# Kernel optimization log

Measured on AMD Instinct MI355X. Metric: run time of the kernel, lower is better.

Reference implementation:

```python
import jax, jax.numpy as jnp
import numpy as np

B, N, D, H = 2, 2048, 1024, 16
HD = D // H  # 64
EPS = 1e-6


def setup_inputs() -> dict:
    key = jax.random.key(0)
    ks = jax.random.split(key, 16)
    rnd = lambda k, shp: jax.random.normal(k, shp, dtype=jnp.float32)
    w = lambda k, i, o: rnd(k, (i, o)) * 0.02  # stored as (in, out); y = x @ W
    return {
        "x": rnd(ks[0], (B, N, D)),
        "emb_B_D": rnd(ks[1], (B, D)),
        "gate": rnd(ks[2], (B, D)),
        "crossattn_emb": rnd(ks[3], (B, 128, D)),
        "rope_emb_L_1_1_D": rnd(ks[4], (N, HD)),
        "Wq1": w(ks[5], D, D), "Wq2": w(ks[6], D, D),
        "Wk1": w(ks[7], D, D), "Wk2": w(ks[8], D, D),
        "Wv": w(ks[9], D, D),
        "Wo": w(ks[10], D, D),
        "Wada1": w(ks[11], D, D),
        "Wada2": w(ks[12], D, 2 * D),
        "bada2": jnp.zeros((2 * D,), dtype=jnp.float32),
    }


def rotate_half(t):
    t1, t2 = jnp.split(t, 2, axis=-1)
    return jnp.concatenate([-t2, t1], axis=-1)


def reference(x, emb_B_D, gate, crossattn_emb, rope_emb_L_1_1_D,
              Wq1, Wq2, Wk1, Wk2, Wv, Wo, Wada1, Wada2, bada2):
    # adaLN modulation: SiLU -> Linear(no bias) -> Linear(bias)
    ada = jax.nn.silu(emb_B_D) @ Wada1 @ Wada2 + bada2          # [B, 2D]
    shift, scale = jnp.split(ada, 2, axis=1)                    # [B, D] each

    # LayerNorm (no affine) + scale/shift
    mu = jnp.mean(x, axis=-1, keepdims=True)
    var = jnp.var(x, axis=-1, keepdims=True)
    xn = (x - mu) * jax.lax.rsqrt(var + EPS)
    xn = xn * (1.0 + scale[:, None, :]) + shift[:, None, :]     # [B, N, D]

    # QKV projections (each to_q/to_k is two stacked linears, to_v one)
    q = xn @ Wq1 @ Wq2
    k = xn @ Wk1 @ Wk2
    v = xn @ Wv
    split_heads = lambda t: t.reshape(B, N, H, HD).transpose(0, 2, 1, 3)  # b h n d
    q, k, v = split_heads(q), split_heads(k), split_heads(v)

    # RoPE
    cos = jnp.cos(rope_emb_L_1_1_D)[None, None]                 # [1,1,N,HD]
    sin = jnp.sin(rope_emb_L_1_1_D)[None, None]
    q = q * cos + rotate_half(q) * sin
    k = k * cos + rotate_half(k) * sin

    # Attention
    sim = jnp.einsum("bhid,bhjd->bhij", q, k) * (HD ** -0.5)
    attn = jax.nn.softmax(sim, axis=-1)
    out = jnp.einsum("bhij,bhjd->bhid", attn, v)
    out = out.transpose(0, 2, 1, 3).reshape(B, N, D) @ Wo

    # Gated residual
    return x + gate[:, None, :] * out
```

## Files before the change

### kernel.cpp

```cpp
#include <hip/hip_runtime.h>
#include <stdint.h>
#include <math.h>

typedef unsigned short u16;
typedef __attribute__((ext_vector_type(8))) short short8;
typedef __attribute__((ext_vector_type(4))) float f32x4;
typedef __attribute__((ext_vector_type(4))) unsigned short u16x4;
typedef __attribute__((ext_vector_type(2))) unsigned int uint2v;

#define DEV static __device__ __forceinline__

DEV u16 f2bf(float f) {
    unsigned u = __builtin_bit_cast(unsigned, f);
    u = u + 0x7fffu + ((u >> 16) & 1u);
    return (u16)(u >> 16);
}
DEV float bf2f(u16 s) { return __builtin_bit_cast(float, ((unsigned)s) << 16); }
DEV float fexp2(float x) {
#if __has_builtin(__builtin_amdgcn_exp2f)
    return __builtin_amdgcn_exp2f(x);
#else
    return __expf(x * 0.69314718056f);
#endif
}
DEV unsigned cvtpk(float a, float b) {
    unsigned w;
    asm("v_cvt_pk_bf16_f32 %0, %1, %2" : "=v"(w) : "v"(a), "v"(b));
    return w;
}
DEV int xcd_swz(int flat, int nwg) {
    int cpx = nwg >> 3;
    return (flat & 7) * cpx + (flat >> 3);
}

DEV void gl_lds16(const u16* g, u16* l) {
#if __has_builtin(__builtin_amdgcn_global_load_lds)
    __builtin_amdgcn_global_load_lds((const __attribute__((address_space(1))) unsigned int*)g,
                                     (__attribute__((address_space(3))) unsigned int*)l, 16, 0, 0);
#else
    *(short8*)l = *(const short8*)g;
#endif
}

DEV void barrier_lgkm() {
    asm volatile("s_waitcnt lgkmcnt(0)" ::: "memory");
    __builtin_amdgcn_sched_barrier(0);
    __builtin_amdgcn_s_barrier();
}


__global__ __launch_bounds__(256) void k_ada1(const float* __restrict__ emb, const float* __restrict__ W,
                                              float* __restrict__ out) {
    int col = blockIdx.x * 64 + (threadIdx.x & 63);
    int b = blockIdx.y;
    int kbase = blockIdx.z * 128 + (threadIdx.x >> 6) * 32;
    float acc = 0.f;
    for (int k = kbase; k < kbase + 32; k++) {
        float e = emb[b * 1024 + k];
        float se = e / (1.f + __expf(-e));
        acc += se * W[(size_t)k * 1024 + col];
    }
    __shared__ float red[4][64];
    red[threadIdx.x >> 6][threadIdx.x & 63] = acc;
    __syncthreads();
    if (threadIdx.x < 64)
        atomicAdd(out + b * 1024 + blockIdx.x * 64 + threadIdx.x,
                  red[0][threadIdx.x] + red[1][threadIdx.x] + red[2][threadIdx.x] + red[3][threadIdx.x]);
}

__global__ __launch_bounds__(256) void k_prep(const float* s0, u16* d0, const float* s1, u16* d1,
                                              const float* s2, u16* d2, const float* s3, u16* d3,
                                              const float* s4, u16* d4, const float* s5, u16* d5,
                                              const float* __restrict__ t_ada, const float* __restrict__ Wada2,
                                              float* __restrict__ ada, const float* __restrict__ rope,
                                              float* __restrict__ cst, float* __restrict__ snt) {
    __shared__ u16 tile[64][65];
    __shared__ float red[4][64];
    if (blockIdx.z == 6) {
        int flat = blockIdx.y * 16 + blockIdx.x;
        int kq = flat >> 6;
        int rest = flat & 63;
        int b = rest >> 5, xb = rest & 31;
        int col = xb * 64 + (threadIdx.x & 63);
        int kbase = kq * 256 + (threadIdx.x >> 6) * 64;
        float acc = 0.f;
        for (int k = kbase; k < kbase + 64; k++)
            acc += t_ada[b * 1024 + k] * Wada2[(size_t)k * 2048 + col];
        red[threadIdx.x >> 6][threadIdx.x & 63] = acc;
        __syncthreads();
        if (threadIdx.x < 64)
            atomicAdd(ada + b * 2048 + xb * 64 + threadIdx.x,
                      red[0][threadIdx.x] + red[1][threadIdx.x] + red[2][threadIdx.x] + red[3][threadIdx.x]);
        return;
    }
    if (blockIdx.z == 7) {
        int flat = blockIdx.y * 16 + blockIdx.x;
        if (flat < 128) {
            int idx = flat * 1024 + threadIdx.x * 4;
            float4 rv = *(const float4*)(rope + idx);
            float4 cv, sv;
            __sincosf(rv.x, &sv.x, &cv.x);
            __sincosf(rv.y, &sv.y, &cv.y);
            __sincosf(rv.z, &sv.z, &cv.z);
            __sincosf(rv.w, &sv.w, &cv.w);
            *(float4*)(cst + idx) = cv;
            *(float4*)(snt + idx) = sv;
        }
        return;
    }
    const float* s; u16* d;
    switch (blockIdx.z) {
        case 0: s = s0; d = d0; break;
        case 1: s = s1; d = d1; break;
        case 2: s = s2; d = d2; break;
        case 3: s = s3; d = d3; break;
        case 4: s = s4; d = d4; break;
        default: s = s5; d = d5; break;
    }
    int k0 = blockIdx.x * 64, n0 = blockIdx.y * 64;
    int tx = threadIdx.x & 63, ty = threadIdx.x >> 6;
    if (blockIdx.z >= 4) {
        #pragma unroll
        for (int i = 0; i < 16; i++) {
            int kk = ty + 4 * i;
            d[(size_t)(k0 + kk) * 1024 + n0 + tx] = f2bf(s[(size_t)(k0 + kk) * 1024 + n0 + tx]);
        }
        return;
    }
    #pragma unroll
    for (int i = 0; i < 16; i++) {
        int kk = ty + 4 * i;
        tile[kk][tx] = f2bf(s[(size_t)(k0 + kk) * 1024 + n0 + tx]);
    }
    __syncthreads();
    #pragma unroll
    for (int i = 0; i < 16; i++) {
        int nn = ty + 4 * i;
        d[(size_t)(n0 + nn) * 1024 + k0 + tx] = tile[tx][nn];
    }
}

__global__ __launch_bounds__(256) void k_ln(const float* __restrict__ x, const float* __restrict__ ada,
                                            const float* __restrict__ bada2, u16* __restrict__ xn) {
    int row = blockIdx.x;
    int b = row >> 11;
    float4 v = ((const float4*)(x + (size_t)row * 1024))[threadIdx.x];
    float s = v.x + v.y + v.z + v.w;
    float ss = v.x * v.x + v.y * v.y + v.z * v.z + v.w * v.w;
    #pragma unroll
    for (int m = 1; m < 64; m <<= 1) { s += __shfl_xor(s, m, 64); ss += __shfl_xor(ss, m, 64); }
    __shared__ float red[2][4];
    int wave = threadIdx.x >> 6, lane = threadIdx.x & 63;
    if (lane == 0) { red[0][wave] = s; red[1][wave] = ss; }
    __syncthreads();
    s = red[0][0] + red[0][1] + red[0][2] + red[0][3];
    ss = red[1][0] + red[1][1] + red[1][2] + red[1][3];
    float mu = s * (1.f / 1024.f);
    float var = ss * (1.f / 1024.f) - mu * mu;
    float rs = rsqrtf(var + 1e-6f);
    int c = threadIdx.x * 4;
    const float* sh = ada + b * 2048;
    const float* sc = ada + b * 2048 + 1024;
    u16x4 r;
    r.x = f2bf((v.x - mu) * rs * (1.f + sc[c + 0] + bada2[1024 + c + 0]) + sh[c + 0] + bada2[c + 0]);
    r.y = f2bf((v.y - mu) * rs * (1.f + sc[c + 1] + bada2[1024 + c + 1]) + sh[c + 1] + bada2[c + 1]);
    r.z = f2bf((v.z - mu) * rs * (1.f + sc[c + 2] + bada2[1024 + c + 2]) + sh[c + 2] + bada2[c + 2]);
    r.w = f2bf((v.w - mu) * rs * (1.f + sc[c + 3] + bada2[1024 + c + 3]) + sh[c + 3] + bada2[c + 3]);
    *(u16x4*)(xn + (size_t)row * 1024 + c) = r;
}

template <int BM, int BN, int MODE>
DEV void gemm_core(const u16* __restrict__ A, const u16* __restrict__ Bt,
                   u16* __restrict__ Cb, float* __restrict__ Cf, u16* __restrict__ Vt,
                   const float* __restrict__ Xres, const float* __restrict__ gate,
                   const float* __restrict__ cst, const float* __restrict__ snt,
                   float scale, int Nn, int K, int m0, int n0) {
    constexpr int MI = BM / 32, NJ = BN / 32;
    constexpr int PA = BM / 64, PB = BN / 64;
    constexpr int LA = BM * 32, LB = BN * 32;
    constexpr int LBUF = LA + LB;
    constexpr int SST = 3 * LBUF;
    constexpr int SM = (MODE == 2 && BM * 132 > SST) ? BM * 132 : SST;
    __shared__ u16 smem[SM];
    int tid = threadIdx.x;
    int lane = tid & 63, wave = tid >> 6;
    int wm = (wave & 1) * (BM / 2), wn = (wave >> 1) * (BN / 2);
    int lr = lane & 15, quad = lane >> 4;
    f32x4 acc[MI][NJ];
    #pragma unroll
    for (int i = 0; i < MI; i++)
        #pragma unroll
        for (int j = 0; j < NJ; j++) acc[i][j] = f32x4{0.f, 0.f, 0.f, 0.f};

    int arow = tid >> 2;
    int achunk = (tid & 3) * 8;
    const u16* ap = A + (size_t)(m0 + arow) * K + achunk;
    const u16* bp = Bt + (size_t)(n0 + arow) * K + achunk;

    auto stage = [&](int it, int d) {
        int koff = it * 32;
        int ab = d * LBUF, bb = d * LBUF + LA;
        #pragma unroll
        for (int p = 0; p < PA; p++)
            gl_lds16(ap + koff + (size_t)(64 * p) * K, smem + ab + (arow + 64 * p) * 32 + achunk);
        #pragma unroll
        for (int p = 0; p < PB; p++)
            gl_lds16(bp + koff + (size_t)(64 * p) * K, smem + bb + (arow + 64 * p) * 32 + achunk);
    };

    stage(0, 0);
    stage(1, 1);
    asm volatile("s_waitcnt vmcnt(%0)" :: "i"(PA + PB) : "memory");
    __builtin_amdgcn_sched_barrier(0);
    __builtin_amdgcn_s_barrier();
    #pragma unroll 1
    for (int it = 0; it < 32; ++it) {
        int cur = it % 3;
        if (it + 2 < 32) stage(it + 2, (it + 2) % 3);
        int ab = cur * LBUF, bb = ab + LA;
        short8 af[MI], bfr[NJ];
        #pragma unroll
        for (int i = 0; i < MI; i++)
            af[i] = *(const short8*)(smem + ab + (wm + i * 16 + lr) * 32 + quad * 8);
        #pragma unroll
        for (int j = 0; j < NJ; j++)
            bfr[j] = *(const short8*)(smem + bb + (wn + j * 16 + lr) * 32 + quad * 8);
        #pragma unroll
        for (int i = 0; i < MI; i++)
            #pragma unroll
            for (int j = 0; j < NJ; j++)
                acc[i][j] = __builtin_amdgcn_mfma_f32_16x16x32_bf16(af[i], bfr[j], acc[i][j], 0, 0, 0);
        if (it + 1 < 32) {
            if (it + 2 < 32)
                asm volatile("s_waitcnt vmcnt(%0)" :: "i"(PA + PB) : "memory");
            else
                asm volatile("s_waitcnt vmcnt(0)" ::: "memory");
            __builtin_amdgcn_sched_barrier(0);
            __builtin_amdgcn_s_barrier();
        }
    }
    __syncthreads();

    if (MODE == 2) {
        if ((n0 + wn) < 2048) {
            #pragma unroll
            for (int i = 0; i < MI; i++)
                #pragma unroll
                for (int jp = 0; jp < 2; jp++)
                    #pragma unroll
                    for (int r = 0; r < 4; r++) {
                        int row = m0 + wm + i * 16 + quad * 4 + r;
                        int n = row & 2047;
                        int d1 = jp * 16 + lr;
                        float c1 = cst[n * 64 + d1],      s1 = snt[n * 64 + d1];
                        float c2 = cst[n * 64 + d1 + 32], s2 = snt[n * 64 + d1 + 32];
                        float x1 = acc[i][jp][r], x2 = acc[i][jp + 2][r];
                        Cb[(size_t)row * Nn + n0 + wn + d1]      = f2bf(x1 * c1 - x2 * s1);
                        Cb[(size_t)row * Nn + n0 + wn + d1 + 32] = f2bf(x2 * c2 + x1 * s2);
                    }
        } else {
            #pragma unroll
            for (int i = 0; i < MI; i++)
                #pragma unroll
                for (int j = 0; j < NJ; j++) {
                    u16x4 w;
                    w.x = f2bf(acc[i][j][0]); w.y = f2bf(acc[i][j][1]);
                    w.z = f2bf(acc[i][j][2]); w.w = f2bf(acc[i][j][3]);
                    *(u16x4*)(&smem[(wn + j * 16 + lr) * 132 + wm + i * 16 + quad * 4]) = w;
                }
            __syncthreads();
            int d = tid >> 1, half = tid & 1;
            int gcol = n0 - 2048 + d;
            int hv = gcol >> 6, dl = gcol & 63;
            int bb2 = m0 >> 11;
            int nloc = (m0 & 2047) + half * 64;
            u16* dst = Vt + ((size_t)((bb2 * 16 + hv) * 64 + dl)) * 2048 + nloc;
            #pragma unroll
            for (int c = 0; c < 8; c++)
                *(short8*)(dst + c * 8) = *(const short8*)(&smem[d * 132 + half * 64 + c * 8]);
        }
        return;
    }
    #pragma unroll
    for (int i = 0; i < MI; i++)
        #pragma unroll
        for (int j = 0; j < NJ; j++)
            #pragma unroll
            for (int r = 0; r < 4; r++) {
                int row = m0 + wm + i * 16 + quad * 4 + r;
                int col = n0 + wn + j * 16 + lr;
                float v = acc[i][j][r];
                if (MODE == 1) {
                    int b = row >> 11;
                    Cf[(size_t)row * Nn + col] = Xres[(size_t)row * Nn + col] + gate[b * 1024 + col] * v;
                } else {
                    Cb[(size_t)row * Nn + col] = f2bf(v * scale);
                }
            }
}

template <int BM, int BN, int MODE, int WPE>
__global__ __launch_bounds__(256, WPE) void gemm_bt(const u16* __restrict__ A, const u16* __restrict__ Bt,
                                                    u16* __restrict__ Cb, float* __restrict__ Cf,
                                                    u16* __restrict__ Vt,
                                                    const float* __restrict__ Xres, const float* __restrict__ gate,
                                                    const float* __restrict__ cst, const float* __restrict__ snt,
                                                    int Nn, int K) {
    int gx = gridDim.x;
    int flat = blockIdx.y * gx + blockIdx.x;
    int swz = xcd_swz(flat, gx * gridDim.y);
    gemm_core<BM, BN, MODE>(A, Bt, Cb, Cf, Vt, Xres, gate, cst, snt, 1.f, Nn, K,
                            (swz / gx) * BM, (swz % gx) * BN);
}

__global__ __launch_bounds__(256, 4) void gemm_fold(const u16* A0, const u16* B0, u16* C0,
                                                    const u16* A1, const u16* B1, u16* C1) {
    const u16* A = blockIdx.z ? A1 : A0;
    const u16* Bt = blockIdx.z ? B1 : B0;
    u16* C = blockIdx.z ? C1 : C0;
    float scale = blockIdx.z ? 1.0f : 0.18033688f;
    int flat = blockIdx.y * 16 + blockIdx.x;
    int swz = xcd_swz(flat, 128);
    gemm_core<128, 64, 0>(A, Bt, C, nullptr, nullptr, nullptr, nullptr, nullptr, nullptr, scale,
                          1024, 1024, (swz >> 4) * 128, (swz & 15) * 64);
}

__global__ __launch_bounds__(512) void k_attn(const u16* __restrict__ qkv, const u16* __restrict__ vt,
                                              u16* __restrict__ aob) {
    __shared__ u16 pool[128 * 72];
    __shared__ u16 Ks[2][64][64];
    __shared__ u16 Vs[2][64][64];
    int flat = blockIdx.y * 16 + blockIdx.x;
    int swz = xcd_swz(flat, 512);
    int q0 = (swz & 15) * 128;
    int bh = swz >> 4; int b = bh >> 4, h = bh & 15;
    int tid = threadIdx.x;
    int lane = tid & 63, wave = tid >> 6;
    int lr = lane & 15, quad = lane >> 4;
    int srow = tid >> 3, scol = (tid & 7) * 8;
    int sg = (((tid & 7) ^ (srow & 7))) * 8;
    int cc[2] = { ((quad ^ (lr & 7))) * 8, (((4 + quad) ^ (lr & 7))) * 8 };
    int qrow = wave * 16 + lr;

    const u16* kp = qkv + ((size_t)(b * 2048 + srow)) * 2048 + 1024 + h * 64 + sg;
    const u16* vp = vt + ((size_t)(bh * 64 + srow)) * 2048 + sg;

    #pragma unroll
    for (int p = 0; p < 2; p++)
        gl_lds16(qkv + ((size_t)(b * 2048 + q0 + srow + 64 * p)) * 2048 + h * 64 + sg,
                 pool + (srow + 64 * p) * 64 + scol);

    short8 krA, vrA, krB, vrB;
    krA = *(const short8*)(kp);
    vrA = *(const short8*)(vp);
    __syncthreads();
    short8 qf[2];
    #pragma unroll
    for (int ks = 0; ks < 2; ks++)
        qf[ks] = *(const short8*)(pool + qrow * 64 + cc[ks]);
    *(short8*)(&Ks[0][srow][scol]) = krA;
    *(short8*)(&Vs[0][srow][scol]) = vrA;
    krB = *(const short8*)(kp + (size_t)64 * 2048);
    vrB = *(const short8*)(vp + 64);
    __syncthreads();

    float l_part = 0.f;
    f32x4 oacc[4];
    #pragma unroll
    for (int dt = 0; dt < 4; dt++) oacc[dt] = f32x4{0.f, 0.f, 0.f, 0.f};

    auto body = [&](int it, int cur, short8& krF, short8& vrF, short8& krH, short8& vrH) {
        if (it < 30) {
            krF = *(const short8*)(kp + (size_t)(it + 2) * 64 * 2048);
            vrF = *(const short8*)(vp + (it + 2) * 64);
        }
        f32x4 st[4];
        #pragma unroll
        for (int ct = 0; ct < 4; ct++) st[ct] = f32x4{0.f, 0.f, 0.f, 0.f};
        #pragma unroll
        for (int ks = 0; ks < 2; ks++) {
            short8 kf[4];
            #pragma unroll
            for (int ct = 0; ct < 4; ct++)
                kf[ct] = *(const short8*)(&Ks[cur][ct * 16 + lr][cc[ks]]);
            __builtin_amdgcn_s_setprio(1);
            #pragma unroll
            for (int ct = 0; ct < 4; ct++)
                st[ct] = __builtin_amdgcn_mfma_f32_16x16x32_bf16(kf[ct], qf[ks], st[ct], 0, 0, 0);
            __builtin_amdgcn_s_setprio(0);
        }
        #pragma unroll
        for (int ct = 0; ct < 4; ct++) {
            float p0 = fexp2(st[ct][0]);
            float p1 = fexp2(st[ct][1]);
            float p2 = fexp2(st[ct][2]);
            float p3 = fexp2(st[ct][3]);
            l_part += (p0 + p1) + (p2 + p3);
            uint2v w; w.x = cvtpk(p0, p1); w.y = cvtpk(p2, p3);
            *(uint2v*)(pool + qrow * 72 + ct * 16 + quad * 4) = w;
        }
        #pragma unroll
        for (int ks = 0; ks < 2; ks++) {
            short8 pf, vf[4];
            pf = *(const short8*)(pool + qrow * 72 + ks * 32 + quad * 8);
            #pragma unroll
            for (int dt = 0; dt < 4; dt++)
                vf[dt] = *(const short8*)(&Vs[cur][dt * 16 + lr][cc[ks]]);
            __builtin_amdgcn_s_setprio(1);
            #pragma unroll
            for (int dt = 0; dt < 4; dt++)
                oacc[dt] = __builtin_amdgcn_mfma_f32_16x16x32_bf16(pf, vf[dt], oacc[dt], 0, 0, 0);
            __builtin_amdgcn_s_setprio(0);
        }
        if (it < 31) {
            int nxt = cur ^ 1;
            *(short8*)(&Ks[nxt][srow][scol]) = krH;
            *(short8*)(&Vs[nxt][srow][scol]) = vrH;
        }
        barrier_lgkm();
    };

    #pragma unroll 1
    for (int it2 = 0; it2 < 16; ++it2) {
        body(2 * it2,     0, krA, vrA, krB, vrB);
        body(2 * it2 + 1, 1, krB, vrB, krA, vrA);
    }

    float l = l_part;
    l += __shfl_xor(l, 16, 64);
    l += __shfl_xor(l, 32, 64);
    float linv[4];
    #pragma unroll
    for (int r = 0; r < 4; r++)
        linv[r] = 1.f / __shfl(l, quad * 4 + r, 64);
    #pragma unroll
    for (int dt = 0; dt < 4; dt++)
        #pragma unroll
        for (int r = 0; r < 4; r++) {
            int row = q0 + wave * 16 + quad * 4 + r;
            aob[((size_t)(b * 2048 + row)) * 1024 + h * 64 + dt * 16 + lr] =
                f2bf(oacc[dt][r] * linv[r]);
        }
}

extern "C" void kernel_launch(void* const* d_in, const int* in_sizes, int n_in,
                              void* d_out, int out_size, void* d_ws, size_t ws_size,
                              hipStream_t stream) {
    const float* x     = (const float*)d_in[0];
    const float* emb   = (const float*)d_in[1];
    const float* gate  = (const float*)d_in[2];
    const float* rope  = (const float*)d_in[4];
    const float* Wq1   = (const float*)d_in[5];
    const float* Wq2   = (const float*)d_in[6];
    const float* Wk1   = (const float*)d_in[7];
    const float* Wk2   = (const float*)d_in[8];
    const float* Wv    = (const float*)d_in[9];
    const float* Wo    = (const float*)d_in[10];
    const float* Wada1 = (const float*)d_in[11];
    const float* Wada2 = (const float*)d_in[12];
    const float* bada2 = (const float*)d_in[13];
    float* out = (float*)d_out;

    char* ws = (char*)d_ws;
    size_t off = 0;
    auto alloc = [&](size_t bytes) { void* p = ws + off; off += (bytes + 255) & ~(size_t)255; return p; };
    float* t_ada = (float*)alloc(2048 * 4);
    float* ada   = (float*)alloc(4096 * 4);
    float* cst   = (float*)alloc((size_t)131072 * 4);
    float* snt   = (float*)alloc((size_t)131072 * 4);
    u16* xn    = (u16*)alloc((size_t)4096 * 1024 * 2);
    u16* Wq1b  = (u16*)alloc((size_t)1024 * 1024 * 2);
    u16* Wk1b  = (u16*)alloc((size_t)1024 * 1024 * 2);
    u16* Wq2t  = (u16*)alloc((size_t)1024 * 1024 * 2);
    u16* Wk2t  = (u16*)alloc((size_t)1024 * 1024 * 2);
    u16* Wot   = (u16*)alloc((size_t)1024 * 1024 * 2);
    u16* WqkvT = (u16*)alloc((size_t)3072 * 1024 * 2);
    u16* qkvb  = (u16*)alloc((size_t)4096 * 2048 * 2);
    u16* vtb   = (u16*)alloc((size_t)4096 * 1024 * 2);
    u16* aob   = (u16*)alloc((size_t)4096 * 1024 * 2);
    (void)ws_size; (void)in_sizes; (void)n_in; (void)out_size;

    hipMemsetAsync(t_ada, 0, 2048 * 4, stream);
    hipMemsetAsync(ada, 0, 4096 * 4, stream);

    k_ada1<<<dim3(16, 2, 8), 256, 0, stream>>>(emb, Wada1, t_ada);

    k_prep<<<dim3(16, 16, 8), 256, 0, stream>>>(Wq2, Wq2t, Wk2, Wk2t,
                                                Wv, WqkvT + (size_t)2048 * 1024, Wo, Wot,
                                                Wq1, Wq1b, Wk1, Wk1b,
                                                t_ada, Wada2, ada, rope, cst, snt);

    k_ln<<<4096, 256, 0, stream>>>(x, ada, bada2, xn);

    gemm_fold<<<dim3(16, 8, 2), 256, 0, stream>>>(Wq2t, Wq1b, WqkvT,
                                                  Wk2t, Wk1b, WqkvT + (size_t)1024 * 1024);

    gemm_bt<128, 128, 2, 4><<<dim3(24, 32), 256, 0, stream>>>(xn, WqkvT, qkvb, nullptr, vtb,
                                                              nullptr, nullptr, cst, snt, 2048, 1024);

    k_attn<<<dim3(16, 32), 512, 0, stream>>>(qkvb, vtb, aob);

    gemm_bt<128, 64, 1, 4><<<dim3(16, 32), 256, 0, stream>>>(aob, Wot, nullptr, out, nullptr, x, gate,
                                                             nullptr, nullptr, 1024, 1024);
}
```

Baseline: 257.2 us.

## Fuse weight-fold GEMM with LayerNorm launch and shrink output GEMM tile

Result: no change. 260.3 us (+1.2%).

```diff
diff --git a/kernel.cpp b/kernel.cpp
--- a/kernel.cpp
+++ b/kernel.cpp
@@ -140,9 +140,167 @@
     }
 }
 
-__global__ __launch_bounds__(256) void k_ln(const float* __restrict__ x, const float* __restrict__ ada,
-                                            const float* __restrict__ bada2, u16* __restrict__ xn) {
-    int row = blockIdx.x;
+template <int BM, int BN, int MODE>
+DEV void gemm_core(const u16* __restrict__ A, const u16* __restrict__ Bt,
+                   u16* __restrict__ Cb, float* __restrict__ Cf, u16* __restrict__ Vt,
+                   const float* __restrict__ Xres, const float* __restrict__ gate,
+                   const float* __restrict__ cst, const float* __restrict__ snt,
+                   float scale, int Nn, int K, int m0, int n0) {
+    constexpr int MI = BM / 32, NJ = BN / 32;
+    constexpr int PA = BM / 64, PB = BN / 64;
+    constexpr int LA = BM * 32, LB = BN * 32;
+    constexpr int LBUF = LA + LB;
+    constexpr int SST = 3 * LBUF;
+    constexpr int SM = (MODE == 2 && BM * 132 > SST) ? BM * 132 : SST;
+    __shared__ u16 smem[SM];
+    int tid = threadIdx.x;
+    int lane = tid & 63, wave = tid >> 6;
+    int wm = (wave & 1) * (BM / 2), wn = (wave >> 1) * (BN / 2);
+    int lr = lane & 15, quad = lane >> 4;
+    f32x4 acc[MI][NJ];
+    #pragma unroll
+    for (int i = 0; i < MI; i++)
+        #pragma unroll
+        for (int j = 0; j < NJ; j++) acc[i][j] = f32x4{0.f, 0.f, 0.f, 0.f};
+
+    int arow = tid >> 2;
+    int achunk = (tid & 3) * 8;
+    const u16* ap = A + (size_t)(m0 + arow) * K + achunk;
+    const u16* bp = Bt + (size_t)(n0 + arow) * K + achunk;
+
+    auto stage = [&](int it, int d) {
+        int koff = it * 32;
+        int ab = d * LBUF, bb = d * LBUF + LA;
+        #pragma unroll
+        for (int p = 0; p < PA; p++)
+            gl_lds16(ap + koff + (size_t)(64 * p) * K, smem + ab + (arow + 64 * p) * 32 + achunk);
+        #pragma unroll
+        for (int p = 0; p < PB; p++)
+            gl_lds16(bp + koff + (size_t)(64 * p) * K, smem + bb + (arow + 64 * p) * 32 + achunk);
+    };
+
+    stage(0, 0);
+    stage(1, 1);
+    asm volatile("s_waitcnt vmcnt(%0)" :: "i"(PA + PB) : "memory");
+    __builtin_amdgcn_sched_barrier(0);
+    __builtin_amdgcn_s_barrier();
+    #pragma unroll 1
+    for (int it = 0; it < 32; ++it) {
+        int cur = it % 3;
+        if (it + 2 < 32) stage(it + 2, (it + 2) % 3);
+        int ab = cur * LBUF, bb = ab + LA;
+        short8 af[MI], bfr[NJ];
+        #pragma unroll
+        for (int i = 0; i < MI; i++)
+            af[i] = *(const short8*)(smem + ab + (wm + i * 16 + lr) * 32 + quad * 8);
+        #pragma unroll
+        for (int j = 0; j < NJ; j++)
+            bfr[j] = *(const short8*)(smem + bb + (wn + j * 16 + lr) * 32 + quad * 8);
+        #pragma unroll
+        for (int i = 0; i < MI; i++)
+            #pragma unroll
+            for (int j = 0; j < NJ; j++)
+                acc[i][j] = __builtin_amdgcn_mfma_f32_16x16x32_bf16(af[i], bfr[j], acc[i][j], 0, 0, 0);
+        if (it + 1 < 32) {
+            if (it + 2 < 32)
+                asm volatile("s_waitcnt vmcnt(%0)" :: "i"(PA + PB) : "memory");
+            else
+                asm volatile("s_waitcnt vmcnt(0)" ::: "memory");
+            __builtin_amdgcn_sched_barrier(0);
+            __builtin_amdgcn_s_barrier();
+        }
+    }
+    __syncthreads();
+
+    if (MODE == 2) {
+        if ((n0 + wn) < 2048) {
+            #pragma unroll
+            for (int i = 0; i < MI; i++)
+                #pragma unroll
+                for (int jp = 0; jp < 2; jp++)
+                    #pragma unroll
+                    for (int r = 0; r < 4; r++) {
+                        int row = m0 + wm + i * 16 + quad * 4 + r;
+                        int n = row & 2047;
+                        int d1 = jp * 16 + lr;
+                        float c1 = cst[n * 64 + d1],      s1 = snt[n * 64 + d1];
+                        float c2 = cst[n * 64 + d1 + 32], s2 = snt[n * 64 + d1 + 32];
+                        float x1 = acc[i][jp][r], x2 = acc[i][jp + 2][r];
+                        Cb[(size_t)row * Nn + n0 + wn + d1]      = f2bf(x1 * c1 - x2 * s1);
+                        Cb[(size_t)row * Nn + n0 + wn + d1 + 32] = f2bf(x2 * c2 + x1 * s2);
+                    }
+        } else {
+            #pragma unroll
+            for (int i = 0; i < MI; i++)
+                #pragma unroll
+                for (int j = 0; j < NJ; j++) {
+                    u16x4 w;
+                    w.x = f2bf(acc[i][j][0]); w.y = f2bf(acc[i][j][1]);
+                    w.z = f2bf(acc[i][j][2]); w.w = f2bf(acc[i][j][3]);
+                    *(u16x4*)(&smem[(wn + j * 16 + lr) * 132 + wm + i * 16 + quad * 4]) = w;
+                }
+            __syncthreads();
+            int d = tid >> 1, half = tid & 1;
+            int gcol = n0 - 2048 + d;
+            int hv = gcol >> 6, dl = gcol & 63;
+            int bb2 = m0 >> 11;
+            int nloc = (m0 & 2047) + half * 64;
+            u16* dst = Vt + ((size_t)((bb2 * 16 + hv) * 64 + dl)) * 2048 + nloc;
+            #pragma unroll
+            for (int c = 0; c < 8; c++)
+                *(short8*)(dst + c * 8) = *(const short8*)(&smem[d * 132 + half * 64 + c * 8]);
+        }
+        return;
+    }
+    #pragma unroll
+    for (int i = 0; i < MI; i++)
+        #pragma unroll
+        for (int j = 0; j < NJ; j++)
+            #pragma unroll
+            for (int r = 0; r < 4; r++) {
+                int row = m0 + wm + i * 16 + quad * 4 + r;
+                int col = n0 + wn + j * 16 + lr;
+                float v = acc[i][j][r];
+                if (MODE == 1) {
+                    int b = row >> 11;
+                    Cf[(size_t)row * Nn + col] = Xres[(size_t)row * Nn + col] + gate[b * 1024 + col] * v;
+                } else {
+                    Cb[(size_t)row * Nn + col] = f2bf(v * scale);
+                }
+            }
+}
+
+template <int BM, int BN, int MODE, int WPE>
+__global__ __launch_bounds__(256, WPE) void gemm_bt(const u16* __restrict__ A, const u16* __restrict__ Bt,
+                                                    u16* __restrict__ Cb, float* __restrict__ Cf,
+                                                    u16* __restrict__ Vt,
+                                                    const float* __restrict__ Xres, const float* __restrict__ gate,
+                                                    const float* __restrict__ cst, const float* __restrict__ snt,
+                                                    int Nn, int K) {
+    int gx = gridDim.x;
+    int flat = blockIdx.y * gx + blockIdx.x;
+    int swz = xcd_swz(flat, gx * gridDim.y);
+    gemm_core<BM, BN, MODE>(A, Bt, Cb, Cf, Vt, Xres, gate, cst, snt, 1.f, Nn, K,
+                            (swz / gx) * BM, (swz % gx) * BN);
+}
+
+__global__ __launch_bounds__(256) void k_foldln(const u16* A0, const u16* B0, u16* C0,
+                                                const u16* A1, const u16* B1, u16* C1,
+                                                const float* __restrict__ x, const float* __restrict__ ada,
+                                                const float* __restrict__ bada2, u16* __restrict__ xn) {
+    int fid = blockIdx.x;
+    if (fid < 256) {
+        int z = fid >> 7, flat = fid & 127;
+        int swz = xcd_swz(flat, 128);
+        const u16* A = z ? A1 : A0;
+        const u16* Bt = z ? B1 : B0;
+        u16* C = z ? C1 : C0;
+        float scale = z ? 1.0f : 0.18033688f;
+        gemm_core<128, 64, 0>(A, Bt, C, nullptr, nullptr, nullptr, nullptr, nullptr, nullptr, scale,
+                              1024, 1024, (swz >> 4) * 128, (swz & 15) * 64);
+        return;
+    }
+    int row = fid - 256;
     int b = row >> 11;
     float4 v = ((const float4*)(x + (size_t)row * 1024))[threadIdx.x];
     float s = v.x + v.y + v.z + v.w;
@@ -169,162 +327,6 @@
     *(u16x4*)(xn + (size_t)row * 1024 + c) = r;
 }
 
-template <int BM, int BN, int MODE>
-DEV void gemm_core(const u16* __restrict__ A, const u16* __restrict__ Bt,
-                   u16* __restrict__ Cb, float* __restrict__ Cf, u16* __restrict__ Vt,
-                   const float* __restrict__ Xres, const float* __restrict__ gate,
-                   const float* __restrict__ cst, const float* __restrict__ snt,
-                   float scale, int Nn, int K, int m0, int n0) {
-    constexpr int MI = BM / 32, NJ = BN / 32;
-    constexpr int PA = BM / 64, PB = BN / 64;
-    constexpr int LA = BM * 32, LB = BN * 32;
-    constexpr int LBUF = LA + LB;
-    constexpr int SST = 3 * LBUF;
-    constexpr int SM = (MODE == 2 && BM * 132 > SST) ? BM * 132 : SST;
-    __shared__ u16 smem[SM];
-    int tid = threadIdx.x;
-    int lane = tid & 63, wave = tid >> 6;
-    int wm = (wave & 1) * (BM / 2), wn = (wave >> 1) * (BN / 2);
-    int lr = lane & 15, quad = lane >> 4;
-    f32x4 acc[MI][NJ];
-    #pragma unroll
-    for (int i = 0; i < MI; i++)
-        #pragma unroll
-        for (int j = 0; j < NJ; j++) acc[i][j] = f32x4{0.f, 0.f, 0.f, 0.f};
-
-    int arow = tid >> 2;
-    int achunk = (tid & 3) * 8;
-    const u16* ap = A + (size_t)(m0 + arow) * K + achunk;
-    const u16* bp = Bt + (size_t)(n0 + arow) * K + achunk;
-
-    auto stage = [&](int it, int d) {
-        int koff = it * 32;
-        int ab = d * LBUF, bb = d * LBUF + LA;
-        #pragma unroll
-        for (int p = 0; p < PA; p++)
-            gl_lds16(ap + koff + (size_t)(64 * p) * K, smem + ab + (arow + 64 * p) * 32 + achunk);
-        #pragma unroll
-        for (int p = 0; p < PB; p++)
-            gl_lds16(bp + koff + (size_t)(64 * p) * K, smem + bb + (arow + 64 * p) * 32 + achunk);
-    };
-
-    stage(0, 0);
-    stage(1, 1);
-    asm volatile("s_waitcnt vmcnt(%0)" :: "i"(PA + PB) : "memory");
-    __builtin_amdgcn_sched_barrier(0);
-    __builtin_amdgcn_s_barrier();
-    #pragma unroll 1
-    for (int it = 0; it < 32; ++it) {
-        int cur = it % 3;
-        if (it + 2 < 32) stage(it + 2, (it + 2) % 3);
-        int ab = cur * LBUF, bb = ab + LA;
-        short8 af[MI], bfr[NJ];
-        #pragma unroll
-        for (int i = 0; i < MI; i++)
-            af[i] = *(const short8*)(smem + ab + (wm + i * 16 + lr) * 32 + quad * 8);
-        #pragma unroll
-        for (int j = 0; j < NJ; j++)
-            bfr[j] = *(const short8*)(smem + bb + (wn + j * 16 + lr) * 32 + quad * 8);
-        #pragma unroll
-        for (int i = 0; i < MI; i++)
-            #pragma unroll
-            for (int j = 0; j < NJ; j++)
-                acc[i][j] = __builtin_amdgcn_mfma_f32_16x16x32_bf16(af[i], bfr[j], acc[i][j], 0, 0, 0);
-        if (it + 1 < 32) {
-            if (it + 2 < 32)
-                asm volatile("s_waitcnt vmcnt(%0)" :: "i"(PA + PB) : "memory");
-            else
-                asm volatile("s_waitcnt vmcnt(0)" ::: "memory");
-            __builtin_amdgcn_sched_barrier(0);
-            __builtin_amdgcn_s_barrier();
-        }
-    }
-    __syncthreads();
-
-    if (MODE == 2) {
-        if ((n0 + wn) < 2048) {
-            #pragma unroll
-            for (int i = 0; i < MI; i++)
-                #pragma unroll
-                for (int jp = 0; jp < 2; jp++)
-                    #pragma unroll
-                    for (int r = 0; r < 4; r++) {
-                        int row = m0 + wm + i * 16 + quad * 4 + r;
-                        int n = row & 2047;
-                        int d1 = jp * 16 + lr;
-                        float c1 = cst[n * 64 + d1],      s1 = snt[n * 64 + d1];
-                        float c2 = cst[n * 64 + d1 + 32], s2 = snt[n * 64 + d1 + 32];
-                        float x1 = acc[i][jp][r], x2 = acc[i][jp + 2][r];
-                        Cb[(size_t)row * Nn + n0 + wn + d1]      = f2bf(x1 * c1 - x2 * s1);
-                        Cb[(size_t)row * Nn + n0 + wn + d1 + 32] = f2bf(x2 * c2 + x1 * s2);
-                    }
-        } else {
-            #pragma unroll
-            for (int i = 0; i < MI; i++)
-                #pragma unroll
-                for (int j = 0; j < NJ; j++) {
-                    u16x4 w;
-                    w.x = f2bf(acc[i][j][0]); w.y = f2bf(acc[i][j][1]);
-                    w.z = f2bf(acc[i][j][2]); w.w = f2bf(acc[i][j][3]);
-                    *(u16x4*)(&smem[(wn + j * 16 + lr) * 132 + wm + i * 16 + quad * 4]) = w;
-                }
-            __syncthreads();
-            int d = tid >> 1, half = tid & 1;
-            int gcol = n0 - 2048 + d;
-            int hv = gcol >> 6, dl = gcol & 63;
-            int bb2 = m0 >> 11;
-            int nloc = (m0 & 2047) + half * 64;
-            u16* dst = Vt + ((size_t)((bb2 * 16 + hv) * 64 + dl)) * 2048 + nloc;
-            #pragma unroll
-            for (int c = 0; c < 8; c++)
-                *(short8*)(dst + c * 8) = *(const short8*)(&smem[d * 132 + half * 64 + c * 8]);
-        }
-        return;
-    }
-    #pragma unroll
-    for (int i = 0; i < MI; i++)
-        #pragma unroll
-        for (int j = 0; j < NJ; j++)
-            #pragma unroll
-            for (int r = 0; r < 4; r++) {
-                int row = m0 + wm + i * 16 + quad * 4 + r;
-                int col = n0 + wn + j * 16 + lr;
-                float v = acc[i][j][r];
-                if (MODE == 1) {
-                    int b = row >> 11;
-                    Cf[(size_t)row * Nn + col] = Xres[(size_t)row * Nn + col] + gate[b * 1024 + col] * v;
-                } else {
-                    Cb[(size_t)row * Nn + col] = f2bf(v * scale);
-                }
-            }
-}
-
-template <int BM, int BN, int MODE, int WPE>
-__global__ __launch_bounds__(256, WPE) void gemm_bt(const u16* __restrict__ A, const u16* __restrict__ Bt,
-                                                    u16* __restrict__ Cb, float* __restrict__ Cf,
-                                                    u16* __restrict__ Vt,
-                                                    const float* __restrict__ Xres, const float* __restrict__ gate,
-                                                    const float* __restrict__ cst, const float* __restrict__ snt,
-                                                    int Nn, int K) {
-    int gx = gridDim.x;
-    int flat = blockIdx.y * gx + blockIdx.x;
-    int swz = xcd_swz(flat, gx * gridDim.y);
-    gemm_core<BM, BN, MODE>(A, Bt, Cb, Cf, Vt, Xres, gate, cst, snt, 1.f, Nn, K,
-                            (swz / gx) * BM, (swz % gx) * BN);
-}
-
-__global__ __launch_bounds__(256, 4) void gemm_fold(const u16* A0, const u16* B0, u16* C0,
-                                                    const u16* A1, const u16* B1, u16* C1) {
-    const u16* A = blockIdx.z ? A1 : A0;
-    const u16* Bt = blockIdx.z ? B1 : B0;
-    u16* C = blockIdx.z ? C1 : C0;
-    float scale = blockIdx.z ? 1.0f : 0.18033688f;
-    int flat = blockIdx.y * 16 + blockIdx.x;
-    int swz = xcd_swz(flat, 128);
-    gemm_core<128, 64, 0>(A, Bt, C, nullptr, nullptr, nullptr, nullptr, nullptr, nullptr, scale,
-                          1024, 1024, (swz >> 4) * 128, (swz & 15) * 64);
-}
-
 __global__ __launch_bounds__(512) void k_attn(const u16* __restrict__ qkv, const u16* __restrict__ vt,
                                               u16* __restrict__ aob) {
     __shared__ u16 pool[128 * 72];
@@ -480,8 +482,7 @@
     u16* aob   = (u16*)alloc((size_t)4096 * 1024 * 2);
     (void)ws_size; (void)in_sizes; (void)n_in; (void)out_size;
 
-    hipMemsetAsync(t_ada, 0, 2048 * 4, stream);
-    hipMemsetAsync(ada, 0, 4096 * 4, stream);
+    hipMemsetAsync(t_ada, 0, 24576, stream);
 
     k_ada1<<<dim3(16, 2, 8), 256, 0, stream>>>(emb, Wada1, t_ada);
 
@@ -490,16 +491,15 @@
                                                 Wq1, Wq1b, Wk1, Wk1b,
                                                 t_ada, Wada2, ada, rope, cst, snt);
 
-    k_ln<<<4096, 256, 0, stream>>>(x, ada, bada2, xn);
-
-    gemm_fold<<<dim3(16, 8, 2), 256, 0, stream>>>(Wq2t, Wq1b, WqkvT,
-                                                  Wk2t, Wk1b, WqkvT + (size_t)1024 * 1024);
+    k_foldln<<<4352, 256, 0, stream>>>(Wq2t, Wq1b, WqkvT,
+                                       Wk2t, Wk1b, WqkvT + (size_t)1024 * 1024,
+                                       x, ada, bada2, xn);
 
     gemm_bt<128, 128, 2, 4><<<dim3(24, 32), 256, 0, stream>>>(xn, WqkvT, qkvb, nullptr, vtb,
                                                               nullptr, nullptr, cst, snt, 2048, 1024);
 
     k_attn<<<dim3(16, 32), 512, 0, stream>>>(qkvb, vtb, aob);
 
-    gemm_bt<128, 64, 1, 4><<<dim3(16, 32), 256, 0, stream>>>(aob, Wot, nullptr, out, nullptr, x, gate,
-                                                             nullptr, nullptr, 1024, 1024);
-}
+    gemm_bt<64, 64, 1, 4><<<dim3(16, 64), 256, 0, stream>>>(aob, Wot, nullptr, out, nullptr, x, gate,
+                                                            nullptr, nullptr, 1024, 1024);
+}
```
